# Performance work log

Measured on AMD Instinct MI355X. Metric: run time of the kernel, lower is better.

Reference implementation:

```python
import jax, jax.numpy as jnp
import numpy as np

N, D, K = 100000, 128, 15
LN_EPS = 1e-5

def setup_inputs() -> dict:
    key = jax.random.key(0)
    k1, k2, k3, k4, k5 = jax.random.split(key, 5)
    node_features = jax.random.normal(k1, (N, D), dtype=jnp.float32)
    neighbor_idx = jax.random.randint(k2, (N, K), 0, N, dtype=jnp.int32)
    neighbor_counts = jax.random.randint(k3, (N,), 0, K + 1, dtype=jnp.int32)
    W = jax.random.normal(k4, (D, D), dtype=jnp.float32) / np.sqrt(D)
    b = jax.random.normal(k5, (D,), dtype=jnp.float32) * 0.01
    ln_w = jnp.ones((D,), dtype=jnp.float32)
    ln_b = jnp.zeros((D,), dtype=jnp.float32)
    return {"node_features": node_features, "neighbor_idx": neighbor_idx,
            "neighbor_counts": neighbor_counts, "W": W, "b": b,
            "ln_w": ln_w, "ln_b": ln_b}

def reference(node_features, neighbor_idx, neighbor_counts, W, b, ln_w, ln_b):
    Kn = neighbor_idx.shape[1]
    # validity mask over padded neighbor slots: [N, K]
    mask = (jnp.arange(Kn)[None, :] < neighbor_counts[:, None]).astype(node_features.dtype)
    feats = node_features[neighbor_idx]              # [N, K, D] gather
    cnt = jnp.maximum(neighbor_counts, 1).astype(node_features.dtype)
    agg = jnp.einsum('nkd,nk->nd', feats, mask) / cnt[:, None]  # mean over valid
    transformed = agg @ W.T + b                       # nn.Linear
    combined = node_features + transformed            # residual
    mu = jnp.mean(combined, axis=-1, keepdims=True)
    var = jnp.mean(jnp.square(combined - mu), axis=-1, keepdims=True)
    normed = (combined - mu) * jax.lax.rsqrt(var + LN_EPS) * ln_w + ln_b
    updated = jax.nn.relu(normed)
    has_nbrs = (neighbor_counts > 0)[:, None]
    return jnp.where(has_nbrs, updated, node_features)
```

## Files before the change

### kernel.cpp

```cpp
#include <hip/hip_runtime.h>
#include <stdint.h>

#define N_NODES 100000
#define DF 128
#define K_NBR 15
#define LN_EPS 1e-5f

typedef __attribute__((ext_vector_type(8))) short bf16x8;
typedef __attribute__((ext_vector_type(4))) float f32x4;

static __device__ __forceinline__ unsigned short f2bf(float f) {
    union { float f; uint32_t u; } v; v.f = f;
    uint32_t u = v.u;
    uint32_t r = u + 0x7FFFu + ((u >> 16) & 1u);
    return (unsigned short)(r >> 16);
}

__global__ __launch_bounds__(256, 3)
void nagg_kernel(const float* __restrict__ nf,
                 const int* __restrict__ nbr,
                 const int* __restrict__ cnts,
                 const float* __restrict__ W,
                 const float* __restrict__ bias,
                 const float* __restrict__ lnw,
                 const float* __restrict__ lnb,
                 float* __restrict__ out)
{
    __shared__ __align__(16) unsigned char smem[32768 + 16384];
    unsigned char* Wb = smem;
    unsigned char* At = smem + 32768;

    const int tid  = threadIdx.x;
    const int lane = tid & 63;
    const int w    = tid >> 6;
    const int base = blockIdx.x * 64;

    {
        const float4* W4 = (const float4*)W;
        #pragma unroll
        for (int it = 0; it < 16; ++it) {
            int e = it * 1024 + tid * 4;
            float4 v = W4[e >> 2];
            int n = e >> 7;
            int k = e & 127;
            ushort4 h;
            h.x = f2bf(v.x); h.y = f2bf(v.y); h.z = f2bf(v.z); h.w = f2bf(v.w);
            int byte = (n * 256 + k * 2) ^ ((n & 7) << 4);
            *(ushort4*)(Wb + byte) = h;
        }
    }

    {
        const int g = lane >> 4;
        const int s = lane & 15;
        for (int t = 0; t < 16; ++t) {
            int m = w * 16 + t;
            int i = base + m;
            bool valid = (i < N_NODES);
            int cnt = valid ? cnts[i] : 0;
            int myidx = (valid && lane < K_NBR) ? nbr[i * K_NBR + lane] : 0;

            float acc[8] = {0.f,0.f,0.f,0.f,0.f,0.f,0.f,0.f};
            #pragma unroll
            for (int st = 0; st < 4; ++st) {
                int k = st * 4 + g;
                int idx = __shfl(myidx, k & 15);
                if (k < cnt) {
                    const float4* p = (const float4*)(nf + (size_t)idx * DF + s * 8);
                    float4 u0 = p[0];
                    float4 u1 = p[1];
                    acc[0]+=u0.x; acc[1]+=u0.y; acc[2]+=u0.z; acc[3]+=u0.w;
                    acc[4]+=u1.x; acc[5]+=u1.y; acc[6]+=u1.z; acc[7]+=u1.w;
                }
            }
            #pragma unroll
            for (int j = 0; j < 8; ++j) {
                acc[j] += __shfl_xor(acc[j], 16);
                acc[j] += __shfl_xor(acc[j], 32);
            }
            if (g == 0) {
                float inv = 1.0f / (float)(cnt > 0 ? cnt : 1);
                uint4 pk;
                pk.x = (uint)f2bf(acc[0]*inv) | ((uint)f2bf(acc[1]*inv) << 16);
                pk.y = (uint)f2bf(acc[2]*inv) | ((uint)f2bf(acc[3]*inv) << 16);
                pk.z = (uint)f2bf(acc[4]*inv) | ((uint)f2bf(acc[5]*inv) << 16);
                pk.w = (uint)f2bf(acc[6]*inv) | ((uint)f2bf(acc[7]*inv) << 16);
                int byte = (m * 256 + s * 16) ^ ((m & 7) << 4);
                *(uint4*)(At + byte) = pk;
            }
        }
    }

    __syncthreads();

    const int l15 = lane & 15;
    const int q   = lane >> 4;

    bf16x8 afr[4];
    #pragma unroll
    for (int kk = 0; kk < 4; ++kk) {
        int m = w * 16 + l15;
        int byte = (m * 256 + kk * 64 + q * 16) ^ ((m & 7) << 4);
        afr[kk] = *(const bf16x8*)(At + byte);
    }

    f32x4 acc[8];
    #pragma unroll
    for (int nb = 0; nb < 8; ++nb) acc[nb] = (f32x4){0.f,0.f,0.f,0.f};

    #pragma unroll
    for (int nb = 0; nb < 8; ++nb) {
        #pragma unroll
        for (int kk = 0; kk < 4; ++kk) {
            int n = nb * 16 + l15;
            int byte = (n * 256 + kk * 64 + q * 16) ^ ((n & 7) << 4);
            bf16x8 bfr = *(const bf16x8*)(Wb + byte);
            acc[nb] = __builtin_amdgcn_mfma_f32_16x16x32_bf16(afr[kk], bfr, acc[nb], 0, 0, 0);
        }
    }

    float bv[8], lwv[8], lbv[8];
    #pragma unroll
    for (int nb = 0; nb < 8; ++nb) {
        int c = nb * 16 + l15;
        bv[nb]  = bias[c];
        lwv[nb] = lnw[c];
        lbv[nb] = lnb[c];
    }

    #pragma unroll
    for (int r = 0; r < 4; ++r) {
        int mloc = q * 4 + r;
        int node = base + w * 16 + mloc;
        if (node < N_NODES) {
            int cnt = cnts[node];
            float vals[8], nfv[8];
            float s = 0.f, sq = 0.f;
            #pragma unroll
            for (int nb = 0; nb < 8; ++nb) {
                int c = nb * 16 + l15;
                float nv = nf[(size_t)node * DF + c];
                float comb = nv + acc[nb][r] + bv[nb];
                nfv[nb]  = nv;
                vals[nb] = comb;
                s  += comb;
                sq += comb * comb;
            }
            #pragma unroll
            for (int off = 1; off < 16; off <<= 1) {
                s  += __shfl_xor(s,  off);
                sq += __shfl_xor(sq, off);
            }
            float mu   = s  * (1.0f / 128.0f);
            float var  = sq * (1.0f / 128.0f) - mu * mu;
            float rstd = rsqrtf(var + LN_EPS);
            #pragma unroll
            for (int nb = 0; nb < 8; ++nb) {
                int c = nb * 16 + l15;
                float nrm = (vals[nb] - mu) * rstd * lwv[nb] + lbv[nb];
                float rel = fmaxf(nrm, 0.0f);
                out[(size_t)node * DF + c] = (cnt > 0) ? rel : nfv[nb];
            }
        }
    }
}

extern "C" void kernel_launch(void* const* d_in, const int* in_sizes, int n_in,
                              void* d_out, int out_size, void* d_ws, size_t ws_size,
                              hipStream_t stream) {
    const float* nf   = (const float*)d_in[0];
    const int*   nbr  = (const int*)d_in[1];
    const int*   cnts = (const int*)d_in[2];
    const float* W    = (const float*)d_in[3];
    const float* b    = (const float*)d_in[4];
    const float* lnw  = (const float*)d_in[5];
    const float* lnb  = (const float*)d_in[6];
    float* out = (float*)d_out;

    int blocks = (N_NODES + 63) / 64;
    nagg_kernel<<<blocks, 256, 0, stream>>>(nf, nbr, cnts, W, b, lnw, lnb, out);
}
```

Measured before the change: 194.5 us.

## Stage neighbor indices and counts in LDS and double nodes per block

Each block now handles 128 nodes with 512 threads, so the bf16 conversion of W into LDS is spread over twice as many nodes. Up front, each wave loads its rows' counts and neighbor indices into LDS with batched loads. This replaces the per-node global loads and shuffles inside the gather loop, which the loop is also unrolled by 2 to overlap. The cost is about 73KB of LDS per block, which limits how many blocks fit on a CU and may reduce occupancy.

Result: faster. 173.5 us (-10.8%).

```diff
diff --git a/kernel.cpp b/kernel.cpp
--- a/kernel.cpp
+++ b/kernel.cpp
@@ -1,9 +1,9 @@
 #include <hip/hip_runtime.h>
 #include <stdint.h>
 
-#define N_NODES 100000
+#define NN 100000
 #define DF 128
-#define K_NBR 15
+#define KN 15
 #define LN_EPS 1e-5f
 
 typedef __attribute__((ext_vector_type(8))) short bf16x8;
@@ -11,12 +11,11 @@
 
 static __device__ __forceinline__ unsigned short f2bf(float f) {
     union { float f; uint32_t u; } v; v.f = f;
-    uint32_t u = v.u;
-    uint32_t r = u + 0x7FFFu + ((u >> 16) & 1u);
+    uint32_t r = v.u + 0x7FFFu + ((v.u >> 16) & 1u);
     return (unsigned short)(r >> 16);
 }
 
-__global__ __launch_bounds__(256, 3)
+__global__ __launch_bounds__(512, 4)
 void nagg_kernel(const float* __restrict__ nf,
                  const int* __restrict__ nbr,
                  const int* __restrict__ cnts,
@@ -26,45 +25,60 @@
                  const float* __restrict__ lnb,
                  float* __restrict__ out)
 {
-    __shared__ __align__(16) unsigned char smem[32768 + 16384];
-    unsigned char* Wb = smem;
-    unsigned char* At = smem + 32768;
+    __shared__ __align__(16) unsigned char WbS[32768];
+    __shared__ __align__(16) unsigned char AtS[32768];
+    __shared__ int idxS[128 * 16];
+    __shared__ int cntS[128];
 
     const int tid  = threadIdx.x;
     const int lane = tid & 63;
     const int w    = tid >> 6;
-    const int base = blockIdx.x * 64;
+    const int base = blockIdx.x * 128;
 
     {
         const float4* W4 = (const float4*)W;
         #pragma unroll
-        for (int it = 0; it < 16; ++it) {
-            int e = it * 1024 + tid * 4;
+        for (int it = 0; it < 8; ++it) {
+            int e = it * 2048 + tid * 4;
             float4 v = W4[e >> 2];
             int n = e >> 7;
             int k = e & 127;
             ushort4 h;
             h.x = f2bf(v.x); h.y = f2bf(v.y); h.z = f2bf(v.z); h.w = f2bf(v.w);
-            int byte = (n * 256 + k * 2) ^ ((n & 7) << 4);
-            *(ushort4*)(Wb + byte) = h;
+            *(ushort4*)(WbS + ((n * 256 + k * 2) ^ ((n & 7) << 4))) = h;
+        }
+    }
+
+    {
+        if (lane < 16) {
+            int m = w * 16 + lane;
+            int node = base + m;
+            cntS[m] = (node < NN) ? cnts[node] : 0;
+        }
+        #pragma unroll
+        for (int it = 0; it < 4; ++it) {
+            int e = it * 64 + lane;
+            if (e < 240) {
+                int mm = e / 15, kk = e - mm * 15;
+                int m = w * 16 + mm;
+                int node = base + m;
+                idxS[m * 16 + kk] = (node < NN) ? nbr[(size_t)node * KN + kk] : 0;
+            }
         }
     }
 
     {
         const int g = lane >> 4;
         const int s = lane & 15;
+        #pragma unroll 2
         for (int t = 0; t < 16; ++t) {
             int m = w * 16 + t;
-            int i = base + m;
-            bool valid = (i < N_NODES);
-            int cnt = valid ? cnts[i] : 0;
-            int myidx = (valid && lane < K_NBR) ? nbr[i * K_NBR + lane] : 0;
-
+            int cnt = cntS[m];
             float acc[8] = {0.f,0.f,0.f,0.f,0.f,0.f,0.f,0.f};
             #pragma unroll
             for (int st = 0; st < 4; ++st) {
                 int k = st * 4 + g;
-                int idx = __shfl(myidx, k & 15);
+                int idx = idxS[m * 16 + (k & 15)];
                 if (k < cnt) {
                     const float4* p = (const float4*)(nf + (size_t)idx * DF + s * 8);
                     float4 u0 = p[0];
@@ -85,8 +99,7 @@
                 pk.y = (uint)f2bf(acc[2]*inv) | ((uint)f2bf(acc[3]*inv) << 16);
                 pk.z = (uint)f2bf(acc[4]*inv) | ((uint)f2bf(acc[5]*inv) << 16);
                 pk.w = (uint)f2bf(acc[6]*inv) | ((uint)f2bf(acc[7]*inv) << 16);
-                int byte = (m * 256 + s * 16) ^ ((m & 7) << 4);
-                *(uint4*)(At + byte) = pk;
+                *(uint4*)(AtS + ((m * 256 + s * 16) ^ ((m & 7) << 4))) = pk;
             }
         }
     }
@@ -100,8 +113,7 @@
     #pragma unroll
     for (int kk = 0; kk < 4; ++kk) {
         int m = w * 16 + l15;
-        int byte = (m * 256 + kk * 64 + q * 16) ^ ((m & 7) << 4);
-        afr[kk] = *(const bf16x8*)(At + byte);
+        afr[kk] = *(const bf16x8*)(AtS + ((m * 256 + kk * 64 + q * 16) ^ ((m & 7) << 4)));
     }
 
     f32x4 acc[8];
@@ -113,8 +125,7 @@
         #pragma unroll
         for (int kk = 0; kk < 4; ++kk) {
             int n = nb * 16 + l15;
-            int byte = (n * 256 + kk * 64 + q * 16) ^ ((n & 7) << 4);
-            bf16x8 bfr = *(const bf16x8*)(Wb + byte);
+            bf16x8 bfr = *(const bf16x8*)(WbS + ((n * 256 + kk * 64 + q * 16) ^ ((n & 7) << 4)));
             acc[nb] = __builtin_amdgcn_mfma_f32_16x16x32_bf16(afr[kk], bfr, acc[nb], 0, 0, 0);
         }
     }
@@ -131,9 +142,10 @@
     #pragma unroll
     for (int r = 0; r < 4; ++r) {
         int mloc = q * 4 + r;
-        int node = base + w * 16 + mloc;
-        if (node < N_NODES) {
-            int cnt = cnts[node];
+        int m = w * 16 + mloc;
+        int node = base + m;
+        if (node < NN) {
+            int cnt = cntS[m];
             float vals[8], nfv[8];
             float s = 0.f, sq = 0.f;
             #pragma unroll
@@ -177,6 +189,6 @@
     const float* lnb  = (const float*)d_in[6];
     float* out = (float*)d_out;
 
-    int blocks = (N_NODES + 63) / 64;
-    nagg_kernel<<<blocks, 256, 0, stream>>>(nf, nbr, cnts, W, b, lnw, lnb, out);
+    int blocks = (NN + 127) / 128;
+    nagg_kernel<<<blocks, 512, 0, stream>>>(nf, nbr, cnts, W, b, lnw, lnb, out);
 }
```
